# Performance work log

Measured on AMD Instinct MI355X. Metric: run time of the kernel, lower is better.

The kernel has to match this reference:

```python
import jax, jax.numpy as jnp
import numpy as np

T, HID, HQ, HKV, D = 2048, 4096, 32, 8, 128
ROPE_BASE = 10000.0


def setup_inputs() -> dict:
    key = jax.random.key(0)
    ks = jax.random.split(key, 5)
    scale = 0.02
    hidden_states = jax.random.normal(ks[0], (T, HID), dtype=jnp.float32)
    position_ids = jnp.arange(T, dtype=jnp.int32)
    # HF-style rotary tables: freqs duplicated along last dim -> [T, D]
    inv_freq = 1.0 / (ROPE_BASE ** (jnp.arange(0, D, 2, dtype=jnp.float32) / D))
    ang = position_ids.astype(jnp.float32)[:, None] * inv_freq[None, :]  # [T, D/2]
    emb = jnp.concatenate([ang, ang], axis=-1)  # [T, D]
    cos, sin = jnp.cos(emb), jnp.sin(emb)
    Wq = jax.random.normal(ks[1], (HID, HQ * D), dtype=jnp.float32) * scale
    Wk = jax.random.normal(ks[2], (HID, HKV * D), dtype=jnp.float32) * scale
    Wv = jax.random.normal(ks[3], (HID, HKV * D), dtype=jnp.float32) * scale
    Wo = jax.random.normal(ks[4], (HQ * D, HID), dtype=jnp.float32) * scale
    return {"hidden_states": hidden_states, "position_ids": position_ids,
            "cos": cos, "sin": sin, "Wq": Wq, "Wk": Wk, "Wv": Wv, "Wo": Wo}


def _rotate_half(x):
    x1, x2 = jnp.split(x, 2, axis=-1)
    return jnp.concatenate([-x2, x1], axis=-1)


def reference(hidden_states, position_ids, cos, sin, Wq, Wk, Wv, Wo):
    t = hidden_states.shape[0]
    scaling = D ** -0.5
    # QKV projections (attention_bias=False)
    q = (hidden_states @ Wq).reshape(t, HQ, D)   # [T, Hq, D]
    k = (hidden_states @ Wk).reshape(t, HKV, D)  # [T, Hkv, D]
    v = (hidden_states @ Wv).reshape(t, HKV, D)
    # RoPE: cos/sin [T, D] broadcast over heads
    c, s = cos[:, None, :], sin[:, None, :]
    q = q * c + _rotate_half(q) * s
    k = k * c + _rotate_half(k) * s
    # GQA: expand KV heads to query heads
    groups = HQ // HKV
    k = jnp.repeat(k, groups, axis=1)  # [T, Hq, D]
    v = jnp.repeat(v, groups, axis=1)
    # Causal attention
    scores = jnp.einsum('thd,shd->hts', q, k) * scaling  # [Hq, T, T]
    causal = jnp.tril(jnp.ones((t, t), dtype=bool))
    scores = jnp.where(causal[None], scores, jnp.finfo(scores.dtype).min)
    probs = jax.nn.softmax(scores, axis=-1)
    attn = jnp.einsum('hts,shd->thd', probs, v).reshape(t, HQ * D)
    return attn @ Wo
```

## Files before the change

kernel.cpp:

```cpp
#include <hip/hip_runtime.h>
#include <hip/hip_bf16.h>
#include <cstdint>
#include <cstddef>

#define T_DIM   2048
#define HID     4096
#define HQ      32
#define HKV     8
#define D_HEAD  128
#define QKV_N   6144
#define KOFF    4096
#define VOFF    5120

typedef __attribute__((ext_vector_type(8))) short short8;
typedef __attribute__((ext_vector_type(4))) float floatx4;

__device__ __forceinline__ ushort f2bf(float f) {
    union { float f; uint u; } v; v.f = f;
    uint r = v.u + 0x7fffu + ((v.u >> 16) & 1u);
    return (ushort)(r >> 16);
}
__device__ __forceinline__ float bf2f(ushort h) {
    union { uint u; float f; } v; v.u = ((uint)h) << 16; return v.f;
}
__device__ __forceinline__ short8 ld8(const ushort* p) {
    uint2 a = *(const uint2*)p, b = *(const uint2*)(p + 4);
    union { uint u[4]; short8 s; } x;
    x.u[0] = a.x; x.u[1] = a.y; x.u[2] = b.x; x.u[3] = b.y;
    return x.s;
}
__device__ __forceinline__ void gld_lds16(const ushort* g, ushort* l) {
    __builtin_amdgcn_global_load_lds(
        (__attribute__((address_space(1))) void*)(g),
        (__attribute__((address_space(3))) void*)(l), 16, 0, 0);
}

__global__ void cast_f32_bf16(const float* __restrict__ in, ushort* __restrict__ out, int n) {
    int i = (blockIdx.x * blockDim.x + threadIdx.x) * 4;
    if (i < n) {
        float4 v = *(const float4*)(in + i);
        ushort4 o;
        o.x = f2bf(v.x); o.y = f2bf(v.y); o.z = f2bf(v.z); o.w = f2bf(v.w);
        *(ushort4*)(out + i) = o;
    }
}

__global__ __launch_bounds__(256) void transpose_cast(const float* __restrict__ W,
                                                      ushort* __restrict__ Wt, int K, int N) {
    __shared__ ushort tile[64][72];
    int n0 = blockIdx.x * 64, k0 = blockIdx.y * 64;
    int tx = threadIdx.x & 15, ty = threadIdx.x >> 4;
#pragma unroll
    for (int i = 0; i < 4; i++) {
        int r = ty + i * 16;
        float4 v = *(const float4*)&W[(size_t)(k0 + r) * N + n0 + tx * 4];
        tile[tx * 4 + 0][r] = f2bf(v.x);
        tile[tx * 4 + 1][r] = f2bf(v.y);
        tile[tx * 4 + 2][r] = f2bf(v.z);
        tile[tx * 4 + 3][r] = f2bf(v.w);
    }
    __syncthreads();
#pragma unroll
    for (int i = 0; i < 2; i++) {
        int task = i * 256 + threadIdx.x;
        int nr = task >> 3, c = task & 7;
        short8 o = *(const short8*)&tile[nr][c * 8];
        *(short8*)&Wt[(size_t)(n0 + nr) * K + k0 + c * 8] = o;
    }
}

__global__ void transpose_v(const ushort* __restrict__ qkv, ushort* __restrict__ VtG) {
    __shared__ ushort tile[32][33];
    int t0 = blockIdx.x * 32, d0 = blockIdx.y * 32, kvh = blockIdx.z;
    int tx = threadIdx.x & 31, ty = threadIdx.x >> 5;
#pragma unroll
    for (int i = 0; i < 4; i++) {
        int t = t0 + ty + i * 8;
        tile[ty + i * 8][tx] = qkv[(size_t)t * QKV_N + VOFF + kvh * D_HEAD + d0 + tx];
    }
    __syncthreads();
#pragma unroll
    for (int i = 0; i < 4; i++) {
        int d = d0 + ty + i * 8;
        VtG[((size_t)kvh * D_HEAD + d) * T_DIM + t0 + tx] = tile[tx][ty + i * 8];
    }
}

template <typename OutT>
__global__ __launch_bounds__(256) void gemm_bt(const ushort* __restrict__ A,
                                               const ushort* __restrict__ Bt,
                                               OutT* __restrict__ C,
                                               int K, int lda, int ldb, int ldc) {
    __shared__ ushort As[2][128 * 32];
    __shared__ ushort Bs[2][128 * 32];
    int tid = threadIdx.x;
    int w = tid >> 6, lane = tid & 63, quad = lane >> 4, l15 = lane & 15;
    int wr = (w >> 1) * 64, wc = (w & 1) * 64;
    int bid = blockIdx.x;
    int xb = ((bid & 7) << 1) | ((bid >> 3) & 1);
    int yb = bid >> 4;
    int m0 = xb * 128, n0 = yb * 128;

    floatx4 acc[4][4];
    floatx4 z = {0.f, 0.f, 0.f, 0.f};
#pragma unroll
    for (int i = 0; i < 4; i++)
#pragma unroll
        for (int j = 0; j < 4; j++) acc[i][j] = z;

    int arow = tid >> 2, ac = (tid & 3) * 8;
    const ushort* gA0 = A + (size_t)(m0 + arow) * lda + ac;
    const ushort* gA1 = A + (size_t)(m0 + arow + 64) * lda + ac;
    const ushort* gB0 = Bt + (size_t)(n0 + arow) * ldb + ac;
    const ushort* gB1 = Bt + (size_t)(n0 + arow + 64) * ldb + ac;

    gld_lds16(gA0, &As[0][tid * 8]);
    gld_lds16(gA1, &As[0][64 * 32 + tid * 8]);
    gld_lds16(gB0, &Bs[0][tid * 8]);
    gld_lds16(gB1, &Bs[0][64 * 32 + tid * 8]);
    gA0 += 32; gA1 += 32; gB0 += 32; gB1 += 32;

    int cur = 0;
    for (int k0 = 0; k0 < K; k0 += 32, cur ^= 1) {
        __syncthreads();
        if (k0 + 32 < K) {
            gld_lds16(gA0, &As[cur ^ 1][tid * 8]);
            gld_lds16(gA1, &As[cur ^ 1][64 * 32 + tid * 8]);
            gld_lds16(gB0, &Bs[cur ^ 1][tid * 8]);
            gld_lds16(gB1, &Bs[cur ^ 1][64 * 32 + tid * 8]);
            gA0 += 32; gA1 += 32; gB0 += 32; gB1 += 32;
        }

        short8 af[4];
#pragma unroll
        for (int i = 0; i < 4; i++)
            af[i] = *(const short8*)&As[cur][(wr + i * 16 + l15) * 32 + quad * 8];
#pragma unroll
        for (int j = 0; j < 4; j++) {
            short8 bf = *(const short8*)&Bs[cur][(wc + j * 16 + l15) * 32 + quad * 8];
#pragma unroll
            for (int i = 0; i < 4; i++)
                acc[i][j] = __builtin_amdgcn_mfma_f32_16x16x32_bf16(af[i], bf, acc[i][j], 0, 0, 0);
        }
    }

#pragma unroll
    for (int i = 0; i < 4; i++) {
        int row0 = m0 + wr + i * 16 + quad * 4;
#pragma unroll
        for (int j = 0; j < 4; j++) {
            int col = n0 + wc + j * 16 + l15;
#pragma unroll
            for (int r = 0; r < 4; r++) {
                float v = acc[i][j][r];
                if constexpr (sizeof(OutT) == 2)
                    C[(size_t)(row0 + r) * ldc + col] = (OutT)f2bf(v);
                else
                    C[(size_t)(row0 + r) * ldc + col] = v;
            }
        }
    }
}

__global__ __launch_bounds__(320) void rope_kernel(ushort* __restrict__ qkv,
                                                   const float* __restrict__ cosb,
                                                   const float* __restrict__ sinb) {
    int t = blockIdx.x;
    ushort* row = qkv + (size_t)t * QKV_N;
    const float* cr = cosb + (size_t)t * D_HEAD;
    const float* sr = sinb + (size_t)t * D_HEAD;
    int task = threadIdx.x;
    int slice = task >> 3, d8 = (task & 7) * 8;
    int col = slice * 128 + d8;
    short8 a = *(const short8*)&row[col];
    short8 b = *(const short8*)&row[col + 64];
    float4 c0 = *(const float4*)&cr[d8], c1 = *(const float4*)&cr[d8 + 4];
    float4 s0 = *(const float4*)&sr[d8], s1 = *(const float4*)&sr[d8 + 4];
    short8 oa, ob;
#pragma unroll
    for (int j = 0; j < 8; j++) {
        float cs = (j < 4) ? ((j == 0) ? c0.x : (j == 1) ? c0.y : (j == 2) ? c0.z : c0.w)
                           : ((j == 4) ? c1.x : (j == 5) ? c1.y : (j == 6) ? c1.z : c1.w);
        float sn = (j < 4) ? ((j == 0) ? s0.x : (j == 1) ? s0.y : (j == 2) ? s0.z : s0.w)
                           : ((j == 4) ? s1.x : (j == 5) ? s1.y : (j == 6) ? s1.z : s1.w);
        float x0 = bf2f((ushort)a[j]), x1 = bf2f((ushort)b[j]);
        oa[j] = (short)f2bf(x0 * cs - x1 * sn);
        ob[j] = (short)f2bf(x1 * cs + x0 * sn);
    }
    *(short8*)&row[col] = oa;
    *(short8*)&row[col + 64] = ob;
}

#define PS_STRIDE 68

__global__ __launch_bounds__(256, 2) void attn_kernel(const ushort* __restrict__ qkv,
                                                      const ushort* __restrict__ VtG,
                                                      ushort* __restrict__ attn) {
    __shared__ ushort Ks[64 * 128];
    __shared__ ushort Vt[128 * 64];
    __shared__ ushort Ps[128 * PS_STRIDE];

    int bid = blockIdx.x;
    int kvh = bid & 7;
    int s = bid >> 3;
    int qt = 15 - (s >> 2);
    int h = (kvh << 2) | (s & 3);
    int q0 = qt * 128;
    int kbmax = 2 * qt + 1;
    int tid = threadIdx.x, w = tid >> 6, lane = tid & 63, quad = lane >> 4, l15 = lane & 15;

    const ushort* kbase = qkv + (size_t)KOFF + (size_t)kvh * D_HEAD;
    const ushort* vbase = VtG + (size_t)kvh * D_HEAD * T_DIM;

    const ushort* ksrc[4];
    const ushort* vsrc[4];
#pragma unroll
    for (int i = 0; i < 4; i++) {
        int cid = i * 256 + tid;
        int kr = cid >> 4, kp = cid & 15, kc = kp ^ (kr & 15);
        ksrc[i] = kbase + (size_t)kr * QKV_N + kc * 8;
        int vr = cid >> 3, vp = cid & 7, vc = vp ^ (vr & 7);
        vsrc[i] = vbase + (size_t)vr * T_DIM + vc * 8;
    }

#pragma unroll
    for (int i = 0; i < 4; i++) {
        gld_lds16(ksrc[i], &Ks[(i * 256 + tid) * 8]);
        ksrc[i] += (size_t)64 * QKV_N;
    }

    short8 qf[2][4];
#pragma unroll
    for (int s2 = 0; s2 < 2; s2++) {
        const ushort* qrow = qkv + (size_t)(q0 + s2 * 64 + w * 16 + l15) * QKV_N + h * D_HEAD + quad * 8;
#pragma unroll
        for (int ks = 0; ks < 4; ks++)
            qf[s2][ks] = *(const short8*)(qrow + ks * 32);
    }

    floatx4 o[2][8];
    floatx4 z = {0.f, 0.f, 0.f, 0.f};
#pragma unroll
    for (int s2 = 0; s2 < 2; s2++)
#pragma unroll
        for (int j = 0; j < 8; j++) o[s2][j] = z;
    float lsum[2][4] = {{0.f, 0.f, 0.f, 0.f}, {0.f, 0.f, 0.f, 0.f}};

    const float scale_l2e = 0.08838834764831845f * 1.4426950408889634f;
    const float BOUND = 24.0f;

    __syncthreads();

    for (int kb = 0; kb <= kbmax; kb++) {
        bool act0 = (kb <= 2 * qt);

#pragma unroll
        for (int i = 0; i < 4; i++) {
            gld_lds16(vsrc[i], &Vt[(i * 256 + tid) * 8]);
            vsrc[i] += 64;
        }

        floatx4 sc[2][4];
#pragma unroll
        for (int s2 = 0; s2 < 2; s2++)
#pragma unroll
            for (int jt = 0; jt < 4; jt++) sc[s2][jt] = z;
#pragma unroll
        for (int ks = 0; ks < 4; ks++) {
#pragma unroll
            for (int jt = 0; jt < 4; jt++) {
                short8 kf = ld8(&Ks[(jt * 16 + l15) * 128 + (((ks * 4 + quad) ^ l15) * 8)]);
                if (act0)
                    sc[0][jt] = __builtin_amdgcn_mfma_f32_16x16x32_bf16(qf[0][ks], kf, sc[0][jt], 0, 0, 0);
                sc[1][jt] = __builtin_amdgcn_mfma_f32_16x16x32_bf16(qf[1][ks], kf, sc[1][jt], 0, 0, 0);
            }
        }

#pragma unroll
        for (int s2 = 0; s2 < 2; s2++) {
            if (s2 == 0 && !act0) continue;
            bool diag = (kb == 2 * qt + s2);
#pragma unroll
            for (int r = 0; r < 4; r++) {
                int rloc = w * 16 + quad * 4 + r;
#pragma unroll
                for (int jt = 0; jt < 4; jt++) {
                    float v = fmaf(sc[s2][jt][r], scale_l2e, -BOUND);
                    if (diag && (jt * 16 + l15 > rloc)) v = -1e30f;
                    float p = exp2f(v);
                    lsum[s2][r] += p;
                    Ps[(s2 * 64 + rloc) * PS_STRIDE + jt * 16 + l15] = f2bf(p);
                }
            }
        }

        __syncthreads();

        if (kb < kbmax) {
#pragma unroll
            for (int i = 0; i < 4; i++) {
                gld_lds16(ksrc[i], &Ks[(i * 256 + tid) * 8]);
                ksrc[i] += (size_t)64 * QKV_N;
            }
        }

#pragma unroll
        for (int ks2 = 0; ks2 < 2; ks2++) {
            short8 pf0 = ld8(&Ps[(w * 16 + l15) * PS_STRIDE + ks2 * 32 + quad * 8]);
            short8 pf1 = ld8(&Ps[(64 + w * 16 + l15) * PS_STRIDE + ks2 * 32 + quad * 8]);
#pragma unroll
            for (int jt = 0; jt < 8; jt++) {
                short8 vf = ld8(&Vt[(jt * 16 + l15) * 64 + (((ks2 * 4 + quad) ^ (l15 & 7)) * 8)]);
                if (act0)
                    o[0][jt] = __builtin_amdgcn_mfma_f32_16x16x32_bf16(pf0, vf, o[0][jt], 0, 0, 0);
                o[1][jt] = __builtin_amdgcn_mfma_f32_16x16x32_bf16(pf1, vf, o[1][jt], 0, 0, 0);
            }
        }

        __syncthreads();
    }

#pragma unroll
    for (int s2 = 0; s2 < 2; s2++) {
#pragma unroll
        for (int r = 0; r < 4; r++) {
            float l = lsum[s2][r];
#pragma unroll
            for (int mk = 1; mk <= 8; mk <<= 1) l += __shfl_xor(l, mk);
            float inv = 1.f / l;
            int trow = q0 + s2 * 64 + w * 16 + quad * 4 + r;
            ushort* orow = attn + (size_t)trow * (HQ * D_HEAD) + h * D_HEAD;
#pragma unroll
            for (int jt = 0; jt < 8; jt++)
                orow[jt * 16 + l15] = f2bf(o[s2][jt][r] * inv);
        }
    }
}

extern "C" void kernel_launch(void* const* d_in, const int* in_sizes, int n_in,
                              void* d_out, int out_size, void* d_ws, size_t ws_size,
                              hipStream_t stream) {
    const float* hidden = (const float*)d_in[0];
    const float* cosb = (const float*)d_in[2];
    const float* sinb = (const float*)d_in[3];
    const float* Wq = (const float*)d_in[4];
    const float* Wk = (const float*)d_in[5];
    const float* Wv = (const float*)d_in[6];
    const float* Wo = (const float*)d_in[7];
    float* out = (float*)d_out;

    char* ws = (char*)d_ws;
    ushort* hiddenB = (ushort*)(ws);
    ushort* WqkvT   = (ushort*)(ws + (size_t)(16u << 20));
    ushort* WoT     = (ushort*)(ws + (size_t)(64u << 20));
    ushort* qkv     = (ushort*)(ws + (size_t)(96u << 20));
    ushort* attnO   = (ushort*)(ws + (size_t)(120u << 20));
    ushort* VtG     = (ushort*)(ws + (size_t)(136u << 20));

    cast_f32_bf16<<<8192, 256, 0, stream>>>(hidden, hiddenB, T_DIM * HID);
    transpose_cast<<<dim3(64, 64), 256, 0, stream>>>(Wq, WqkvT, HID, 4096);
    transpose_cast<<<dim3(16, 64), 256, 0, stream>>>(Wk, WqkvT + (size_t)4096 * HID, HID, 1024);
    transpose_cast<<<dim3(16, 64), 256, 0, stream>>>(Wv, WqkvT + (size_t)5120 * HID, HID, 1024);
    transpose_cast<<<dim3(64, 64), 256, 0, stream>>>(Wo, WoT, HID, 4096);

    gemm_bt<ushort><<<768, 256, 0, stream>>>(hiddenB, WqkvT, qkv,
                                             HID, HID, HID, QKV_N);
    rope_kernel<<<T_DIM, 320, 0, stream>>>(qkv, cosb, sinb);
    transpose_v<<<dim3(64, 4, 8), 256, 0, stream>>>(qkv, VtG);
    attn_kernel<<<512, 256, 0, stream>>>(qkv, VtG, attnO);
    gemm_bt<float><<<512, 256, 0, stream>>>(attnO, WoT, out,
                                            HID, HID, HID, HID);
}
```

Measured before the change: 536.8 us.

## Fuse RoPE and V transpose into QKV GEMM epilogue; merge preprocessing launches

The five cast/transpose launches are merged into one preprocessing kernel that dispatches on block index. The QKV GEMM now stages its output tile in shared memory and applies RoPE to Q/K tiles, or writes the transposed V directly, in its epilogue. This removes the separate rope and transpose_v kernels and their extra global reads and writes of qkv, at the cost of a larger shared-memory epilogue and a V path that no longer writes V into qkv. That path is safe only if attention reads V solely from VtG.

Result: faster. 515.6 us (-4.0%).

```diff
diff --git a/kernel.cpp b/kernel.cpp
--- a/kernel.cpp
+++ b/kernel.cpp
@@ -35,21 +35,42 @@
         (__attribute__((address_space(3))) void*)(l), 16, 0, 0);
 }
 
-__global__ void cast_f32_bf16(const float* __restrict__ in, ushort* __restrict__ out, int n) {
-    int i = (blockIdx.x * blockDim.x + threadIdx.x) * 4;
-    if (i < n) {
-        float4 v = *(const float4*)(in + i);
+__global__ __launch_bounds__(256) void preproc(const float* __restrict__ hidden,
+                                               ushort* __restrict__ hiddenB,
+                                               const float* __restrict__ Wq,
+                                               const float* __restrict__ Wk,
+                                               const float* __restrict__ Wv,
+                                               const float* __restrict__ Wo,
+                                               ushort* __restrict__ WqkvT,
+                                               ushort* __restrict__ WoT) {
+    __shared__ ushort tile[64][72];
+    int bid = blockIdx.x, tid = threadIdx.x;
+
+    if (bid < 8192) {
+        int i = (bid * 256 + tid) * 4;
+        float4 v = *(const float4*)(hidden + i);
         ushort4 o;
         o.x = f2bf(v.x); o.y = f2bf(v.y); o.z = f2bf(v.z); o.w = f2bf(v.w);
-        *(ushort4*)(out + i) = o;
-    }
-}
-
-__global__ __launch_bounds__(256) void transpose_cast(const float* __restrict__ W,
-                                                      ushort* __restrict__ Wt, int K, int N) {
-    __shared__ ushort tile[64][72];
-    int n0 = blockIdx.x * 64, k0 = blockIdx.y * 64;
-    int tx = threadIdx.x & 15, ty = threadIdx.x >> 4;
+        *(ushort4*)(hiddenB + i) = o;
+        return;
+    }
+
+    const float* W; ushort* Wt; int N, n0, k0;
+    if (bid < 12288) {
+        int r = bid - 8192;  W = Wq; Wt = WqkvT;                         N = 4096;
+        n0 = (r & 63) * 64;  k0 = (r >> 6) * 64;
+    } else if (bid < 13312) {
+        int r = bid - 12288; W = Wk; Wt = WqkvT + (size_t)4096 * HID;    N = 1024;
+        n0 = (r & 15) * 64;  k0 = (r >> 4) * 64;
+    } else if (bid < 14336) {
+        int r = bid - 13312; W = Wv; Wt = WqkvT + (size_t)5120 * HID;    N = 1024;
+        n0 = (r & 15) * 64;  k0 = (r >> 4) * 64;
+    } else {
+        int r = bid - 14336; W = Wo; Wt = WoT;                           N = 4096;
+        n0 = (r & 63) * 64;  k0 = (r >> 6) * 64;
+    }
+
+    int tx = tid & 15, ty = tid >> 4;
 #pragma unroll
     for (int i = 0; i < 4; i++) {
         int r = ty + i * 16;
@@ -62,27 +83,125 @@
     __syncthreads();
 #pragma unroll
     for (int i = 0; i < 2; i++) {
-        int task = i * 256 + threadIdx.x;
+        int task = i * 256 + tid;
         int nr = task >> 3, c = task & 7;
         short8 o = *(const short8*)&tile[nr][c * 8];
-        *(short8*)&Wt[(size_t)(n0 + nr) * K + k0 + c * 8] = o;
-    }
-}
-
-__global__ void transpose_v(const ushort* __restrict__ qkv, ushort* __restrict__ VtG) {
-    __shared__ ushort tile[32][33];
-    int t0 = blockIdx.x * 32, d0 = blockIdx.y * 32, kvh = blockIdx.z;
-    int tx = threadIdx.x & 31, ty = threadIdx.x >> 5;
+        *(short8*)&Wt[(size_t)(n0 + nr) * HID + k0 + c * 8] = o;
+    }
+}
+
+__global__ __launch_bounds__(256) void gemm_qkv_fused(const ushort* __restrict__ A,
+                                                      const ushort* __restrict__ Bt,
+                                                      ushort* __restrict__ qkv,
+                                                      ushort* __restrict__ VtG,
+                                                      const float* __restrict__ cosb,
+                                                      const float* __restrict__ sinb) {
+    struct Stage { ushort As[2][4096]; ushort Bs[2][4096]; };
+    __shared__ union SmU { Stage st; ushort ep[16896]; } sm;
+
+    int tid = threadIdx.x;
+    int w = tid >> 6, lane = tid & 63, quad = lane >> 4, l15 = lane & 15;
+    int wr = (w >> 1) * 64, wc = (w & 1) * 64;
+    int bid = blockIdx.x;
+    int xb = ((bid & 7) << 1) | ((bid >> 3) & 1);
+    int yb = bid >> 4;
+    int m0 = xb * 128, n0 = yb * 128;
+
+    floatx4 acc[4][4];
+    floatx4 z = {0.f, 0.f, 0.f, 0.f};
+#pragma unroll
+    for (int i = 0; i < 4; i++)
+#pragma unroll
+        for (int j = 0; j < 4; j++) acc[i][j] = z;
+
+    int arow = tid >> 2, ac = (tid & 3) * 8;
+    const ushort* gA0 = A + (size_t)(m0 + arow) * HID + ac;
+    const ushort* gA1 = A + (size_t)(m0 + arow + 64) * HID + ac;
+    const ushort* gB0 = Bt + (size_t)(n0 + arow) * HID + ac;
+    const ushort* gB1 = Bt + (size_t)(n0 + arow + 64) * HID + ac;
+
+    gld_lds16(gA0, &sm.st.As[0][tid * 8]);
+    gld_lds16(gA1, &sm.st.As[0][64 * 32 + tid * 8]);
+    gld_lds16(gB0, &sm.st.Bs[0][tid * 8]);
+    gld_lds16(gB1, &sm.st.Bs[0][64 * 32 + tid * 8]);
+    gA0 += 32; gA1 += 32; gB0 += 32; gB1 += 32;
+
+    int cur = 0;
+    for (int k0 = 0; k0 < HID; k0 += 32, cur ^= 1) {
+        __syncthreads();
+        if (k0 + 32 < HID) {
+            gld_lds16(gA0, &sm.st.As[cur ^ 1][tid * 8]);
+            gld_lds16(gA1, &sm.st.As[cur ^ 1][64 * 32 + tid * 8]);
+            gld_lds16(gB0, &sm.st.Bs[cur ^ 1][tid * 8]);
+            gld_lds16(gB1, &sm.st.Bs[cur ^ 1][64 * 32 + tid * 8]);
+            gA0 += 32; gA1 += 32; gB0 += 32; gB1 += 32;
+        }
+
+        short8 af[4];
+#pragma unroll
+        for (int i = 0; i < 4; i++)
+            af[i] = *(const short8*)&sm.st.As[cur][(wr + i * 16 + l15) * 32 + quad * 8];
+#pragma unroll
+        for (int j = 0; j < 4; j++) {
+            short8 bf = *(const short8*)&sm.st.Bs[cur][(wc + j * 16 + l15) * 32 + quad * 8];
+#pragma unroll
+            for (int i = 0; i < 4; i++)
+                acc[i][j] = __builtin_amdgcn_mfma_f32_16x16x32_bf16(af[i], bf, acc[i][j], 0, 0, 0);
+        }
+    }
+
+    __syncthreads();
 #pragma unroll
     for (int i = 0; i < 4; i++) {
-        int t = t0 + ty + i * 8;
-        tile[ty + i * 8][tx] = qkv[(size_t)t * QKV_N + VOFF + kvh * D_HEAD + d0 + tx];
+        int row0 = wr + i * 16 + quad * 4;
+#pragma unroll
+        for (int j = 0; j < 4; j++) {
+            int col = wc + j * 16 + l15;
+#pragma unroll
+            for (int r = 0; r < 4; r++)
+                sm.ep[(row0 + r) * 132 + col] = f2bf(acc[i][j][r]);
+        }
     }
     __syncthreads();
-#pragma unroll
-    for (int i = 0; i < 4; i++) {
-        int d = d0 + ty + i * 8;
-        VtG[((size_t)kvh * D_HEAD + d) * T_DIM + t0 + tx] = tile[tx][ty + i * 8];
+
+    if (yb < 40) {
+        int colbase = (yb < 32) ? yb * 128 : (KOFF + (yb - 32) * 128);
+#pragma unroll
+        for (int it = 0; it < 4; ++it) {
+            int task = it * 256 + tid;
+            int t = task >> 3, d8 = (task & 7) * 8;
+            int tg = m0 + t;
+            short8 a = ld8(&sm.ep[t * 132 + d8]);
+            short8 b = ld8(&sm.ep[t * 132 + 64 + d8]);
+            const float* cr = cosb + (size_t)tg * D_HEAD + d8;
+            const float* sr = sinb + (size_t)tg * D_HEAD + d8;
+            float4 c0 = *(const float4*)cr, c1 = *(const float4*)(cr + 4);
+            float4 s0 = *(const float4*)sr, s1 = *(const float4*)(sr + 4);
+            short8 oa, ob;
+#pragma unroll
+            for (int j = 0; j < 8; j++) {
+                float cs = (j < 4) ? ((j == 0) ? c0.x : (j == 1) ? c0.y : (j == 2) ? c0.z : c0.w)
+                                   : ((j == 4) ? c1.x : (j == 5) ? c1.y : (j == 6) ? c1.z : c1.w);
+                float sn = (j < 4) ? ((j == 0) ? s0.x : (j == 1) ? s0.y : (j == 2) ? s0.z : s0.w)
+                                   : ((j == 4) ? s1.x : (j == 5) ? s1.y : (j == 6) ? s1.z : s1.w);
+                float x0 = bf2f((ushort)a[j]), x1 = bf2f((ushort)b[j]);
+                oa[j] = (short)f2bf(x0 * cs - x1 * sn);
+                ob[j] = (short)f2bf(x1 * cs + x0 * sn);
+            }
+            *(short8*)&qkv[(size_t)tg * QKV_N + colbase + d8] = oa;
+            *(short8*)&qkv[(size_t)tg * QKV_N + colbase + 64 + d8] = ob;
+        }
+    } else {
+        int kvh = yb - 40;
+#pragma unroll
+        for (int it = 0; it < 8; ++it) {
+            int task = it * 256 + tid;
+            int d = task >> 4, tc = (task & 15) * 8;
+            short8 o;
+#pragma unroll
+            for (int j = 0; j < 8; j++) o[j] = (short)sm.ep[(tc + j) * 132 + d];
+            *(short8*)&VtG[((size_t)kvh * D_HEAD + d) * T_DIM + m0 + tc] = o;
+        }
     }
 }
 
@@ -162,35 +281,6 @@
     }
 }
 
-__global__ __launch_bounds__(320) void rope_kernel(ushort* __restrict__ qkv,
-                                                   const float* __restrict__ cosb,
-                                                   const float* __restrict__ sinb) {
-    int t = blockIdx.x;
-    ushort* row = qkv + (size_t)t * QKV_N;
-    const float* cr = cosb + (size_t)t * D_HEAD;
-    const float* sr = sinb + (size_t)t * D_HEAD;
-    int task = threadIdx.x;
-    int slice = task >> 3, d8 = (task & 7) * 8;
-    int col = slice * 128 + d8;
-    short8 a = *(const short8*)&row[col];
-    short8 b = *(const short8*)&row[col + 64];
-    float4 c0 = *(const float4*)&cr[d8], c1 = *(const float4*)&cr[d8 + 4];
-    float4 s0 = *(const float4*)&sr[d8], s1 = *(const float4*)&sr[d8 + 4];
-    short8 oa, ob;
-#pragma unroll
-    for (int j = 0; j < 8; j++) {
-        float cs = (j < 4) ? ((j == 0) ? c0.x : (j == 1) ? c0.y : (j == 2) ? c0.z : c0.w)
-                           : ((j == 4) ? c1.x : (j == 5) ? c1.y : (j == 6) ? c1.z : c1.w);
-        float sn = (j < 4) ? ((j == 0) ? s0.x : (j == 1) ? s0.y : (j == 2) ? s0.z : s0.w)
-                           : ((j == 4) ? s1.x : (j == 5) ? s1.y : (j == 6) ? s1.z : s1.w);
-        float x0 = bf2f((ushort)a[j]), x1 = bf2f((ushort)b[j]);
-        oa[j] = (short)f2bf(x0 * cs - x1 * sn);
-        ob[j] = (short)f2bf(x1 * cs + x0 * sn);
-    }
-    *(short8*)&row[col] = oa;
-    *(short8*)&row[col + 64] = ob;
-}
-
 #define PS_STRIDE 68
 
 __global__ __launch_bounds__(256, 2) void attn_kernel(const ushort* __restrict__ qkv,
@@ -357,17 +447,8 @@
     ushort* attnO   = (ushort*)(ws + (size_t)(120u << 20));
     ushort* VtG     = (ushort*)(ws + (size_t)(136u << 20));
 
-    cast_f32_bf16<<<8192, 256, 0, stream>>>(hidden, hiddenB, T_DIM * HID);
-    transpose_cast<<<dim3(64, 64), 256, 0, stream>>>(Wq, WqkvT, HID, 4096);
-    transpose_cast<<<dim3(16, 64), 256, 0, stream>>>(Wk, WqkvT + (size_t)4096 * HID, HID, 1024);
-    transpose_cast<<<dim3(16, 64), 256, 0, stream>>>(Wv, WqkvT + (size_t)5120 * HID, HID, 1024);
-    transpose_cast<<<dim3(64, 64), 256, 0, stream>>>(Wo, WoT, HID, 4096);
-
-    gemm_bt<ushort><<<768, 256, 0, stream>>>(hiddenB, WqkvT, qkv,
-                                             HID, HID, HID, QKV_N);
-    rope_kernel<<<T_DIM, 320, 0, stream>>>(qkv, cosb, sinb);
-    transpose_v<<<dim3(64, 4, 8), 256, 0, stream>>>(qkv, VtG);
+    preproc<<<18432, 256, 0, stream>>>(hidden, hiddenB, Wq, Wk, Wv, Wo, WqkvT, WoT);
+    gemm_qkv_fused<<<768, 256, 0, stream>>>(hiddenB, WqkvT, qkv, VtG, cosb, sinb);
     attn_kernel<<<512, 256, 0, stream>>>(qkv, VtG, attnO);
-    gemm_bt<float><<<512, 256, 0, stream>>>(attnO, WoT, out,
-                                            HID, HID, HID, HID);
-}
+    gemm_bt<float><<<512, 256, 0, stream>>>(attnO, WoT, out, HID, HID, HID, HID);
+}
```
